# Kernel tuning notes

Measured on AMD Instinct MI355X. Metric: run time of the kernel, lower is better.

The kernel has to match this reference:

```python
import jax, jax.numpy as jnp
import numpy as np

BN_EPS = 1e-5

def binarize_ste(x):
    # sign() in forward; identity (straight-through) in backward, matching the
    # weight.data / input.data hack in BinarizeConv2d.
    return x + jax.lax.stop_gradient(jnp.sign(x) - x)


def setup_inputs() -> dict:
    key = jax.random.key(0)
    k1, k2, k3, k4 = jax.random.split(key, 4)
    N, Cin, H, W = 16, 32, 224, 224
    Cout, K = 32, 3
    x = jax.random.normal(k1, (N, Cin, H, W), dtype=jnp.float32)
    weight = jax.random.normal(k2, (Cout, Cin, K, K), dtype=jnp.float32) * 0.1
    gamma = jax.random.uniform(k3, (Cout,), dtype=jnp.float32, minval=0.5, maxval=1.5)
    beta = jax.random.normal(k4, (Cout,), dtype=jnp.float32) * 0.1
    return {"x": x, "weight": weight, "gamma": gamma, "beta": beta}


def reference(x, weight, gamma, beta):
    # BinarizeConv2d: binarize input iff C != 3, always binarize weights.
    xb = binarize_ste(x) if x.shape[1] != 3 else x
    wb = binarize_ste(weight)
    y = jax.lax.conv_general_dilated(
        xb, wb,
        window_strides=(1, 1),
        padding=((1, 1), (1, 1)),
        dimension_numbers=("NCHW", "OIHW", "NCHW"),
    )  # [N, Cout, H, W]
    # BatchNorm2d in training mode: per-channel batch statistics over (N, H, W).
    mean = jnp.mean(y, axis=(0, 2, 3))
    var = jnp.var(y, axis=(0, 2, 3))
    inv = jax.lax.rsqrt(var + BN_EPS)
    yn = (y - mean[None, :, None, None]) * inv[None, :, None, None]
    return yn * gamma[None, :, None, None] + beta[None, :, None, None]
```

## Files before the change

kernel.cpp:

```cpp
#include <hip/hip_runtime.h>
#include <stdint.h>

#define NB 16
#define CC 32
#define HH 224
#define WWID 224
#define HWS (HH*WWID)
#define NHWT (NB*HWS)
#define STRIPS (NHWT/4)
#define SPI (HWS/4)
#define SPR (WWID/4)

#define PITCH 232
#define PROWS 226
#define IMGW (PITCH*PROWS)

typedef float    f4 __attribute__((ext_vector_type(4)));
typedef unsigned u4 __attribute__((ext_vector_type(4)));
typedef unsigned u2 __attribute__((ext_vector_type(2)));

#define WS_WSIGN 0
#define WS_WNZ   2048
#define WS_BASE  4096
#define WS_FLAGW 5248
#define WS_FLAGZ 5252
#define WS_SSUM  5376
#define WS_SSQ   5632
#define WS_SCALE 5888
#define WS_SHIFT 6016
#define WS_XS    8192
#define WS_XNZ   (8192 + (size_t)NB*IMGW*4)

__global__ void pack_w(const float* __restrict__ w, unsigned* __restrict__ wsg,
                       unsigned* __restrict__ wnz, int* __restrict__ flagw,
                       int* __restrict__ baset) {
    __shared__ unsigned s_sg[288];
    __shared__ int allnz;
    if (threadIdx.x == 0) allnz = 1;
    __syncthreads();
    int k = threadIdx.x;
    if (k < 288) {
        int co = k / 9, tap = k % 9;
        unsigned bits = 0, nz = 0;
        for (int ci = 0; ci < CC; ++ci) {
            float v = w[(co * CC + ci) * 9 + tap];
            bits |= (v > 0.f ? 1u : 0u) << ci;
            nz   |= (v != 0.f ? 1u : 0u) << ci;
        }
        wsg[k] = bits; wnz[k] = nz; s_sg[k] = bits;
        if (nz != 0xffffffffu) atomicAnd(&allnz, 0);
    }
    __syncthreads();
    if (threadIdx.x == 0) *flagw = allnz;
    if (k < 288) {
        int cls = k >> 5, co = k & 31;
        int hc = cls / 3, wc = cls % 3;
        int nv = 0, corr = 0;
        #pragma unroll
        for (int kh = 0; kh < 3; ++kh)
            #pragma unroll
            for (int kw = 0; kw < 3; ++kw) {
                bool inv = (hc == 0 && kh == 0) || (hc == 2 && kh == 2) ||
                           (wc == 0 && kw == 0) || (wc == 2 && kw == 2);
                if (inv) corr += __popc(s_sg[co * 9 + kh * 3 + kw]);
                else     nv++;
            }
        baset[k] = 32 * nv + 2 * corr;
    }
}

__global__ void __launch_bounds__(256) pack_x4(const float* __restrict__ x,
                                               unsigned* __restrict__ xs,
                                               unsigned* __restrict__ xnz,
                                               int* __restrict__ flagz) {
    int t = blockIdx.x * 256 + threadIdx.x;
    int n = t / SPI, rem = t - n * SPI;
    int h = rem / SPR, w0 = (rem - h * SPR) * 4;
    const float* base = x + (size_t)n * CC * HWS + h * WWID + w0;
    unsigned b0=0,b1=0,b2=0,b3=0, z0=0,z1=0,z2=0,z3=0;
    #pragma unroll
    for (int c = 0; c < CC; ++c) {
        f4 v = __builtin_nontemporal_load((const f4*)(base + (size_t)c * HWS));
        b0 |= (v.x > 0.f ? (1u<<c) : 0u);  z0 |= (v.x != 0.f ? (1u<<c) : 0u);
        b1 |= (v.y > 0.f ? (1u<<c) : 0u);  z1 |= (v.y != 0.f ? (1u<<c) : 0u);
        b2 |= (v.z > 0.f ? (1u<<c) : 0u);  z2 |= (v.z != 0.f ? (1u<<c) : 0u);
        b3 |= (v.w > 0.f ? (1u<<c) : 0u);  z3 |= (v.w != 0.f ? (1u<<c) : 0u);
    }
    size_t d = (size_t)n * IMGW + (h + 1) * PITCH + 1 + w0;
    xs[d+0]=b0; xs[d+1]=b1; xs[d+2]=b2; xs[d+3]=b3;
    xnz[d+0]=z0; xnz[d+1]=z1; xnz[d+2]=z2; xnz[d+3]=z3;
    bool hasz = (z0 & z1 & z2 & z3) != 0xffffffffu;
    if (__any(hasz) && (threadIdx.x & 63) == 0) atomicOr(flagz, 1);
}

__device__ __forceinline__ void loadwin(const unsigned* __restrict__ p, unsigned a[6]) {
    u4 lo = *(const u4*)p;
    u2 hi = *(const u2*)(p + 4);
    a[0]=lo.x; a[1]=lo.y; a[2]=lo.z; a[3]=lo.w; a[4]=hi.x; a[5]=hi.y;
}

__device__ __forceinline__ void ad4(const unsigned a0[6], const unsigned a1[6],
                                    const unsigned a2[6],
                                    const unsigned* __restrict__ q, int ad[4]) {
    unsigned q0=q[0],q1=q[1],q2=q[2],q3=q[3],q4=q[4],q5=q[5],q6=q[6],q7=q[7],q8=q[8];
    #pragma unroll
    for (int px = 0; px < 4; ++px) {
        ad[px] = __popc(a0[px]^q0) + __popc(a0[px+1]^q1) + __popc(a0[px+2]^q2)
               + __popc(a1[px]^q3) + __popc(a1[px+1]^q4) + __popc(a1[px+2]^q5)
               + __popc(a2[px]^q6) + __popc(a2[px+1]^q7) + __popc(a2[px+2]^q8);
    }
}

__device__ __forceinline__ void y4_slowc(const unsigned a0[6], const unsigned a1[6],
                                         const unsigned a2[6], const unsigned z0[6],
                                         const unsigned z1[6], const unsigned z2[6],
                                         const unsigned* __restrict__ qs,
                                         const unsigned* __restrict__ qz, int y[4]) {
    #pragma unroll
    for (int px = 0; px < 4; ++px) {
        int am = 0, ad = 0;
        #pragma unroll
        for (int kw = 0; kw < 3; ++kw) {
            unsigned m0 = z0[px+kw] & qz[kw];
            unsigned m1 = z1[px+kw] & qz[3+kw];
            unsigned m2 = z2[px+kw] & qz[6+kw];
            am += __popc(m0) + __popc(m1) + __popc(m2);
            ad += __popc((a0[px+kw]^qs[kw])   & m0)
                + __popc((a1[px+kw]^qs[3+kw]) & m1)
                + __popc((a2[px+kw]^qs[6+kw]) & m2);
        }
        y[px] = am - 2 * ad;
    }
}

__global__ void __launch_bounds__(256, 4) convstats_fast(
        const unsigned* __restrict__ xs, const unsigned* __restrict__ wsg,
        const int* __restrict__ baset, const int* __restrict__ flagw,
        const int* __restrict__ flagz, int* __restrict__ s_sum,
        unsigned long long* __restrict__ s_sq) {
    if (!(*flagw) || *flagz) return;
    __shared__ int sb[288];
    __shared__ int ls[4][8], lq[4][8];
    for (int i = threadIdx.x; i < 288; i += 256) sb[i] = baset[i];
    __syncthreads();

    int cobase = (blockIdx.x & 3) * 8;
    int sid = (blockIdx.x >> 2) * 256 + threadIdx.x;
    int n = sid / SPI, rem = sid - n * SPI;
    int h = rem / SPR, w0 = (rem - h * SPR) * 4;
    const unsigned* ip = xs + (size_t)n * IMGW + h * PITCH + w0;

    unsigned a0[6], a1[6], a2[6];
    loadwin(ip, a0); loadwin(ip + PITCH, a1); loadwin(ip + 2 * PITCH, a2);

    int hc = (h == 0) ? 0 : ((h == HH-1) ? 6 : 3);
    int c0 = (hc + ((w0 == 0) ? 0 : 1)) * 32;
    int c1 = (hc + 1) * 32;
    int c3 = (hc + ((w0 == WWID-4) ? 2 : 1)) * 32;

    int sacc[8], qacc[8];
    #pragma unroll
    for (int u = 0; u < 8; ++u) {
        int co = cobase + u;
        int ad[4];
        ad4(a0, a1, a2, wsg + co * 9, ad);
        int y0 = sb[c0 + co] - 2 * ad[0];
        int y1 = sb[c1 + co] - 2 * ad[1];
        int y2 = sb[c1 + co] - 2 * ad[2];
        int y3 = sb[c3 + co] - 2 * ad[3];
        sacc[u] = y0 + y1 + y2 + y3;
        qacc[u] = y0*y0 + y1*y1 + y2*y2 + y3*y3;
    }

    #pragma unroll
    for (int off = 32; off; off >>= 1) {
        #pragma unroll
        for (int u = 0; u < 8; ++u) {
            sacc[u] += __shfl_down(sacc[u], off);
            qacc[u] += __shfl_down(qacc[u], off);
        }
    }
    int wid = threadIdx.x >> 6, lane = threadIdx.x & 63;
    if (lane == 0) {
        #pragma unroll
        for (int u = 0; u < 8; ++u) { ls[wid][u] = sacc[u]; lq[wid][u] = qacc[u]; }
    }
    __syncthreads();
    if (threadIdx.x < 8) {
        int u = threadIdx.x;
        int S = ls[0][u] + ls[1][u] + ls[2][u] + ls[3][u];
        long long Q = (long long)lq[0][u] + lq[1][u] + lq[2][u] + lq[3][u];
        atomicAdd(&s_sum[cobase + u], S);
        atomicAdd(&s_sq[cobase + u], (unsigned long long)Q);
    }
}

__global__ void __launch_bounds__(256, 2) convstats_slow(
        const unsigned* __restrict__ xs, const unsigned* __restrict__ xnz,
        const unsigned* __restrict__ wsg, const unsigned* __restrict__ wnz,
        const int* __restrict__ flagw, const int* __restrict__ flagz,
        int* __restrict__ s_sum, unsigned long long* __restrict__ s_sq) {
    if ((*flagw) && !(*flagz)) return;
    __shared__ int ls[4][8], lq[4][8];
    int cobase = (blockIdx.x & 3) * 8;
    int sid = (blockIdx.x >> 2) * 256 + threadIdx.x;
    int n = sid / SPI, rem = sid - n * SPI;
    int h = rem / SPR, w0 = (rem - h * SPR) * 4;
    size_t off = (size_t)n * IMGW + h * PITCH + w0;

    unsigned a0[6], a1[6], a2[6], z0[6], z1[6], z2[6];
    loadwin(xs + off, a0); loadwin(xs + off + PITCH, a1); loadwin(xs + off + 2*PITCH, a2);
    loadwin(xnz + off, z0); loadwin(xnz + off + PITCH, z1); loadwin(xnz + off + 2*PITCH, z2);

    int sacc[8], qacc[8];
    #pragma unroll
    for (int u = 0; u < 8; ++u) {
        int co = cobase + u;
        int y[4];
        y4_slowc(a0, a1, a2, z0, z1, z2, wsg + co * 9, wnz + co * 9, y);
        sacc[u] = y[0]+y[1]+y[2]+y[3];
        qacc[u] = y[0]*y[0]+y[1]*y[1]+y[2]*y[2]+y[3]*y[3];
    }
    #pragma unroll
    for (int offv = 32; offv; offv >>= 1) {
        #pragma unroll
        for (int u = 0; u < 8; ++u) {
            sacc[u] += __shfl_down(sacc[u], offv);
            qacc[u] += __shfl_down(qacc[u], offv);
        }
    }
    int wid = threadIdx.x >> 6, lane = threadIdx.x & 63;
    if (lane == 0) {
        #pragma unroll
        for (int u = 0; u < 8; ++u) { ls[wid][u] = sacc[u]; lq[wid][u] = qacc[u]; }
    }
    __syncthreads();
    if (threadIdx.x < 8) {
        int u = threadIdx.x;
        int S = ls[0][u] + ls[1][u] + ls[2][u] + ls[3][u];
        long long Q = (long long)lq[0][u] + lq[1][u] + lq[2][u] + lq[3][u];
        atomicAdd(&s_sum[cobase + u], S);
        atomicAdd(&s_sq[cobase + u], (unsigned long long)Q);
    }
}

__global__ void bfinal(const int* __restrict__ s_sum,
                       const unsigned long long* __restrict__ s_sq,
                       const float* __restrict__ gamma, const float* __restrict__ beta,
                       float* __restrict__ scale, float* __restrict__ shift) {
    int c = threadIdx.x;
    if (c >= CC) return;
    double mean = (double)s_sum[c] / (double)NHWT;
    double var  = (double)(long long)s_sq[c] / (double)NHWT - mean * mean;
    float inv = (float)(1.0 / sqrt(var + 1e-5));
    float g = gamma[c] * inv;
    scale[c] = g;
    shift[c] = beta[c] - (float)mean * g;
}

__global__ void __launch_bounds__(256, 4) convnorm_fast(
        const unsigned* __restrict__ xs, const unsigned* __restrict__ wsg,
        const int* __restrict__ baset, const int* __restrict__ flagw,
        const int* __restrict__ flagz, const float* __restrict__ scale,
        const float* __restrict__ shift, float* __restrict__ out) {
    if (!(*flagw) || *flagz) return;
    __shared__ int sb[288];
    for (int i = threadIdx.x; i < 288; i += 256) sb[i] = baset[i];
    __syncthreads();

    int cobase = (blockIdx.x & 3) * 8;
    int sid = (blockIdx.x >> 2) * 256 + threadIdx.x;
    int n = sid / SPI, rem = sid - n * SPI;
    int h = rem / SPR, w0 = (rem - h * SPR) * 4;
    const unsigned* ip = xs + (size_t)n * IMGW + h * PITCH + w0;

    unsigned a0[6], a1[6], a2[6];
    loadwin(ip, a0); loadwin(ip + PITCH, a1); loadwin(ip + 2 * PITCH, a2);

    int hc = (h == 0) ? 0 : ((h == HH-1) ? 6 : 3);
    int c0 = (hc + ((w0 == 0) ? 0 : 1)) * 32;
    int c1 = (hc + 1) * 32;
    int c3 = (hc + ((w0 == WWID-4) ? 2 : 1)) * 32;

    float* on = out + (size_t)(n * CC + cobase) * HWS + h * WWID + w0;
    #pragma unroll
    for (int u = 0; u < 8; ++u) {
        int co = cobase + u;
        int ad[4];
        ad4(a0, a1, a2, wsg + co * 9, ad);
        int y0 = sb[c0 + co] - 2 * ad[0];
        int y1 = sb[c1 + co] - 2 * ad[1];
        int y2 = sb[c1 + co] - 2 * ad[2];
        int y3 = sb[c3 + co] - 2 * ad[3];
        float sc = scale[co], sh = shift[co];
        f4 o = { fmaf((float)y0, sc, sh), fmaf((float)y1, sc, sh),
                 fmaf((float)y2, sc, sh), fmaf((float)y3, sc, sh) };
        __builtin_nontemporal_store(o, (f4*)(on + (size_t)u * HWS));
    }
}

__global__ void __launch_bounds__(256, 2) convnorm_slow(
        const unsigned* __restrict__ xs, const unsigned* __restrict__ xnz,
        const unsigned* __restrict__ wsg, const unsigned* __restrict__ wnz,
        const int* __restrict__ flagw, const int* __restrict__ flagz,
        const float* __restrict__ scale, const float* __restrict__ shift,
        float* __restrict__ out) {
    if ((*flagw) && !(*flagz)) return;
    int cobase = (blockIdx.x & 3) * 8;
    int sid = (blockIdx.x >> 2) * 256 + threadIdx.x;
    int n = sid / SPI, rem = sid - n * SPI;
    int h = rem / SPR, w0 = (rem - h * SPR) * 4;
    size_t off = (size_t)n * IMGW + h * PITCH + w0;

    unsigned a0[6], a1[6], a2[6], z0[6], z1[6], z2[6];
    loadwin(xs + off, a0); loadwin(xs + off + PITCH, a1); loadwin(xs + off + 2*PITCH, a2);
    loadwin(xnz + off, z0); loadwin(xnz + off + PITCH, z1); loadwin(xnz + off + 2*PITCH, z2);

    float* on = out + (size_t)(n * CC + cobase) * HWS + h * WWID + w0;
    #pragma unroll
    for (int u = 0; u < 8; ++u) {
        int co = cobase + u;
        int y[4];
        y4_slowc(a0, a1, a2, z0, z1, z2, wsg + co * 9, wnz + co * 9, y);
        float sc = scale[co], sh = shift[co];
        f4 o = { fmaf((float)y[0], sc, sh), fmaf((float)y[1], sc, sh),
                 fmaf((float)y[2], sc, sh), fmaf((float)y[3], sc, sh) };
        __builtin_nontemporal_store(o, (f4*)(on + (size_t)u * HWS));
    }
}

extern "C" void kernel_launch(void* const* d_in, const int* in_sizes, int n_in,
                              void* d_out, int out_size, void* d_ws, size_t ws_size,
                              hipStream_t stream) {
    const float* x     = (const float*)d_in[0];
    const float* w     = (const float*)d_in[1];
    const float* gamma = (const float*)d_in[2];
    const float* beta  = (const float*)d_in[3];
    float* out = (float*)d_out;

    char* ws = (char*)d_ws;
    unsigned* wsg            = (unsigned*)(ws + WS_WSIGN);
    unsigned* wnz            = (unsigned*)(ws + WS_WNZ);
    int* baset               = (int*)(ws + WS_BASE);
    int* flagw               = (int*)(ws + WS_FLAGW);
    int* flagz               = (int*)(ws + WS_FLAGZ);
    int* s_sum               = (int*)(ws + WS_SSUM);
    unsigned long long* s_sq = (unsigned long long*)(ws + WS_SSQ);
    float* scale             = (float*)(ws + WS_SCALE);
    float* shift             = (float*)(ws + WS_SHIFT);
    unsigned* xsb            = (unsigned*)(ws + WS_XS);
    unsigned* xzb            = (unsigned*)(ws + WS_XNZ);

    hipMemsetAsync(ws + WS_FLAGZ, 0, WS_SCALE - WS_FLAGZ, stream);
    hipMemsetAsync(ws + WS_XS, 0, (size_t)NB * IMGW * 4 * 2, stream);

    pack_w  <<<1, 320, 0, stream>>>(w, wsg, wnz, flagw, baset);
    pack_x4 <<<STRIPS / 256, 256, 0, stream>>>(x, xsb, xzb, flagz);

    int cgrid = STRIPS / 256 * 4;
    convstats_fast<<<cgrid, 256, 0, stream>>>(xsb, wsg, baset, flagw, flagz, s_sum, s_sq);
    convstats_slow<<<cgrid, 256, 0, stream>>>(xsb, xzb, wsg, wnz, flagw, flagz, s_sum, s_sq);
    bfinal  <<<1, 64, 0, stream>>>(s_sum, s_sq, gamma, beta, scale, shift);
    convnorm_fast<<<cgrid, 256, 0, stream>>>(xsb, wsg, baset, flagw, flagz, scale, shift, out);
    convnorm_slow<<<cgrid, 256, 0, stream>>>(xsb, xzb, wsg, wnz, flagw, flagz, scale, shift, out);
}
```

Measured before the change: 91.72 us.

## Drop memsets and merge fast/slow conv kernels into single launches

Removes the two hipMemsetAsync calls. The stats accumulators and the zero flag are now cleared inside pack_w, and pack_x4 writes the padding border itself, so the large padded-buffer memset is no longer needed. The separate fast and slow conv kernels are merged into one kernel per stage that branches on the flags, cutting two launches, and launch_bounds rises to 8 blocks per CU. In exchange, the merged kernel has to size its registers for the slow path too, and correctness depends on pack_w finishing its clears before pack_x4 sets flagz, which stream order provides.

New measurement: 84.50 us. -7.9%, faster.

```diff
diff --git a/kernel.cpp b/kernel.cpp
--- a/kernel.cpp
+++ b/kernel.cpp
@@ -33,10 +33,12 @@
 
 __global__ void pack_w(const float* __restrict__ w, unsigned* __restrict__ wsg,
                        unsigned* __restrict__ wnz, int* __restrict__ flagw,
-                       int* __restrict__ baset) {
+                       int* __restrict__ baset, int* __restrict__ s_sum,
+                       unsigned long long* __restrict__ s_sq, int* __restrict__ flagz) {
     __shared__ unsigned s_sg[288];
     __shared__ int allnz;
-    if (threadIdx.x == 0) allnz = 1;
+    if (threadIdx.x == 0) { allnz = 1; *flagz = 0; }
+    if (threadIdx.x < CC) { s_sum[threadIdx.x] = 0; s_sq[threadIdx.x] = 0ull; }
     __syncthreads();
     int k = threadIdx.x;
     if (k < 288) {
@@ -86,9 +88,28 @@
         b2 |= (v.z > 0.f ? (1u<<c) : 0u);  z2 |= (v.z != 0.f ? (1u<<c) : 0u);
         b3 |= (v.w > 0.f ? (1u<<c) : 0u);  z3 |= (v.w != 0.f ? (1u<<c) : 0u);
     }
-    size_t d = (size_t)n * IMGW + (h + 1) * PITCH + 1 + w0;
+    size_t rowb = (size_t)n * IMGW + (h + 1) * PITCH;
+    size_t d = rowb + 1 + w0;
     xs[d+0]=b0; xs[d+1]=b1; xs[d+2]=b2; xs[d+3]=b3;
     xnz[d+0]=z0; xnz[d+1]=z1; xnz[d+2]=z2; xnz[d+3]=z3;
+
+    if (w0 == 0)        { xs[rowb] = 0;       xnz[rowb] = 0; }
+    if (w0 == WWID - 4) { xs[rowb + 225] = 0; xnz[rowb + 225] = 0; }
+    if (h == 0) {
+        size_t tr = (size_t)n * IMGW;
+        #pragma unroll
+        for (int j = 0; j < 4; ++j) { xs[tr + 1 + w0 + j] = 0; xnz[tr + 1 + w0 + j] = 0; }
+        if (w0 == 0)        { xs[tr] = 0;       xnz[tr] = 0; }
+        if (w0 == WWID - 4) { xs[tr + 225] = 0; xnz[tr + 225] = 0; }
+    }
+    if (h == HH - 1) {
+        size_t br = (size_t)n * IMGW + (size_t)(PROWS - 1) * PITCH;
+        #pragma unroll
+        for (int j = 0; j < 4; ++j) { xs[br + 1 + w0 + j] = 0; xnz[br + 1 + w0 + j] = 0; }
+        if (w0 == 0)        { xs[br] = 0;       xnz[br] = 0; }
+        if (w0 == WWID - 4) { xs[br + 225] = 0; xnz[br + 225] = 0; }
+    }
+
     bool hasz = (z0 & z1 & z2 & z3) != 0xffffffffu;
     if (__any(hasz) && (threadIdx.x & 63) == 0) atomicOr(flagz, 1);
 }
@@ -133,100 +154,64 @@
     }
 }
 
-__global__ void __launch_bounds__(256, 4) convstats_fast(
-        const unsigned* __restrict__ xs, const unsigned* __restrict__ wsg,
+__global__ void __launch_bounds__(256, 8) convstats(
+        const unsigned* __restrict__ xs, const unsigned* __restrict__ xnz,
+        const unsigned* __restrict__ wsg, const unsigned* __restrict__ wnz,
         const int* __restrict__ baset, const int* __restrict__ flagw,
         const int* __restrict__ flagz, int* __restrict__ s_sum,
         unsigned long long* __restrict__ s_sq) {
-    if (!(*flagw) || *flagz) return;
     __shared__ int sb[288];
     __shared__ int ls[4][8], lq[4][8];
     for (int i = threadIdx.x; i < 288; i += 256) sb[i] = baset[i];
     __syncthreads();
 
-    int cobase = (blockIdx.x & 3) * 8;
-    int sid = (blockIdx.x >> 2) * 256 + threadIdx.x;
-    int n = sid / SPI, rem = sid - n * SPI;
-    int h = rem / SPR, w0 = (rem - h * SPR) * 4;
-    const unsigned* ip = xs + (size_t)n * IMGW + h * PITCH + w0;
-
-    unsigned a0[6], a1[6], a2[6];
-    loadwin(ip, a0); loadwin(ip + PITCH, a1); loadwin(ip + 2 * PITCH, a2);
-
-    int hc = (h == 0) ? 0 : ((h == HH-1) ? 6 : 3);
-    int c0 = (hc + ((w0 == 0) ? 0 : 1)) * 32;
-    int c1 = (hc + 1) * 32;
-    int c3 = (hc + ((w0 == WWID-4) ? 2 : 1)) * 32;
-
-    int sacc[8], qacc[8];
-    #pragma unroll
-    for (int u = 0; u < 8; ++u) {
-        int co = cobase + u;
-        int ad[4];
-        ad4(a0, a1, a2, wsg + co * 9, ad);
-        int y0 = sb[c0 + co] - 2 * ad[0];
-        int y1 = sb[c1 + co] - 2 * ad[1];
-        int y2 = sb[c1 + co] - 2 * ad[2];
-        int y3 = sb[c3 + co] - 2 * ad[3];
-        sacc[u] = y0 + y1 + y2 + y3;
-        qacc[u] = y0*y0 + y1*y1 + y2*y2 + y3*y3;
-    }
-
-    #pragma unroll
-    for (int off = 32; off; off >>= 1) {
-        #pragma unroll
-        for (int u = 0; u < 8; ++u) {
-            sacc[u] += __shfl_down(sacc[u], off);
-            qacc[u] += __shfl_down(qacc[u], off);
-        }
-    }
-    int wid = threadIdx.x >> 6, lane = threadIdx.x & 63;
-    if (lane == 0) {
-        #pragma unroll
-        for (int u = 0; u < 8; ++u) { ls[wid][u] = sacc[u]; lq[wid][u] = qacc[u]; }
-    }
-    __syncthreads();
-    if (threadIdx.x < 8) {
-        int u = threadIdx.x;
-        int S = ls[0][u] + ls[1][u] + ls[2][u] + ls[3][u];
-        long long Q = (long long)lq[0][u] + lq[1][u] + lq[2][u] + lq[3][u];
-        atomicAdd(&s_sum[cobase + u], S);
-        atomicAdd(&s_sq[cobase + u], (unsigned long long)Q);
-    }
-}
-
-__global__ void __launch_bounds__(256, 2) convstats_slow(
-        const unsigned* __restrict__ xs, const unsigned* __restrict__ xnz,
-        const unsigned* __restrict__ wsg, const unsigned* __restrict__ wnz,
-        const int* __restrict__ flagw, const int* __restrict__ flagz,
-        int* __restrict__ s_sum, unsigned long long* __restrict__ s_sq) {
-    if ((*flagw) && !(*flagz)) return;
-    __shared__ int ls[4][8], lq[4][8];
     int cobase = (blockIdx.x & 3) * 8;
     int sid = (blockIdx.x >> 2) * 256 + threadIdx.x;
     int n = sid / SPI, rem = sid - n * SPI;
     int h = rem / SPR, w0 = (rem - h * SPR) * 4;
     size_t off = (size_t)n * IMGW + h * PITCH + w0;
 
-    unsigned a0[6], a1[6], a2[6], z0[6], z1[6], z2[6];
+    unsigned a0[6], a1[6], a2[6];
     loadwin(xs + off, a0); loadwin(xs + off + PITCH, a1); loadwin(xs + off + 2*PITCH, a2);
-    loadwin(xnz + off, z0); loadwin(xnz + off + PITCH, z1); loadwin(xnz + off + 2*PITCH, z2);
 
     int sacc[8], qacc[8];
+    bool fast = (*flagw != 0) && (*flagz == 0);
+    if (fast) {
+        int hc = (h == 0) ? 0 : ((h == HH-1) ? 6 : 3);
+        int c0 = (hc + ((w0 == 0) ? 0 : 1)) * 32;
+        int c1 = (hc + 1) * 32;
+        int c3 = (hc + ((w0 == WWID-4) ? 2 : 1)) * 32;
+        #pragma unroll
+        for (int u = 0; u < 8; ++u) {
+            int co = cobase + u;
+            int ad[4];
+            ad4(a0, a1, a2, wsg + co * 9, ad);
+            int y0 = sb[c0 + co] - 2 * ad[0];
+            int y1 = sb[c1 + co] - 2 * ad[1];
+            int y2 = sb[c1 + co] - 2 * ad[2];
+            int y3 = sb[c3 + co] - 2 * ad[3];
+            sacc[u] = y0 + y1 + y2 + y3;
+            qacc[u] = y0*y0 + y1*y1 + y2*y2 + y3*y3;
+        }
+    } else {
+        unsigned z0[6], z1[6], z2[6];
+        loadwin(xnz + off, z0); loadwin(xnz + off + PITCH, z1); loadwin(xnz + off + 2*PITCH, z2);
+        #pragma unroll
+        for (int u = 0; u < 8; ++u) {
+            int co = cobase + u;
+            int y[4];
+            y4_slowc(a0, a1, a2, z0, z1, z2, wsg + co * 9, wnz + co * 9, y);
+            sacc[u] = y[0]+y[1]+y[2]+y[3];
+            qacc[u] = y[0]*y[0]+y[1]*y[1]+y[2]*y[2]+y[3]*y[3];
+        }
+    }
+
     #pragma unroll
-    for (int u = 0; u < 8; ++u) {
-        int co = cobase + u;
-        int y[4];
-        y4_slowc(a0, a1, a2, z0, z1, z2, wsg + co * 9, wnz + co * 9, y);
-        sacc[u] = y[0]+y[1]+y[2]+y[3];
-        qacc[u] = y[0]*y[0]+y[1]*y[1]+y[2]*y[2]+y[3]*y[3];
-    }
-    #pragma unroll
-    for (int offv = 32; offv; offv >>= 1) {
-        #pragma unroll
-        for (int u = 0; u < 8; ++u) {
-            sacc[u] += __shfl_down(sacc[u], offv);
-            qacc[u] += __shfl_down(qacc[u], offv);
+    for (int off2 = 32; off2; off2 >>= 1) {
+        #pragma unroll
+        for (int u = 0; u < 8; ++u) {
+            sacc[u] += __shfl_down(sacc[u], off2);
+            qacc[u] += __shfl_down(qacc[u], off2);
         }
     }
     int wid = threadIdx.x >> 6, lane = threadIdx.x & 63;
@@ -258,74 +243,59 @@
     shift[c] = beta[c] - (float)mean * g;
 }
 
-__global__ void __launch_bounds__(256, 4) convnorm_fast(
-        const unsigned* __restrict__ xs, const unsigned* __restrict__ wsg,
+__global__ void __launch_bounds__(256, 8) convnorm(
+        const unsigned* __restrict__ xs, const unsigned* __restrict__ xnz,
+        const unsigned* __restrict__ wsg, const unsigned* __restrict__ wnz,
         const int* __restrict__ baset, const int* __restrict__ flagw,
         const int* __restrict__ flagz, const float* __restrict__ scale,
         const float* __restrict__ shift, float* __restrict__ out) {
-    if (!(*flagw) || *flagz) return;
     __shared__ int sb[288];
     for (int i = threadIdx.x; i < 288; i += 256) sb[i] = baset[i];
     __syncthreads();
 
-    int cobase = (blockIdx.x & 3) * 8;
-    int sid = (blockIdx.x >> 2) * 256 + threadIdx.x;
-    int n = sid / SPI, rem = sid - n * SPI;
-    int h = rem / SPR, w0 = (rem - h * SPR) * 4;
-    const unsigned* ip = xs + (size_t)n * IMGW + h * PITCH + w0;
-
-    unsigned a0[6], a1[6], a2[6];
-    loadwin(ip, a0); loadwin(ip + PITCH, a1); loadwin(ip + 2 * PITCH, a2);
-
-    int hc = (h == 0) ? 0 : ((h == HH-1) ? 6 : 3);
-    int c0 = (hc + ((w0 == 0) ? 0 : 1)) * 32;
-    int c1 = (hc + 1) * 32;
-    int c3 = (hc + ((w0 == WWID-4) ? 2 : 1)) * 32;
-
-    float* on = out + (size_t)(n * CC + cobase) * HWS + h * WWID + w0;
-    #pragma unroll
-    for (int u = 0; u < 8; ++u) {
-        int co = cobase + u;
-        int ad[4];
-        ad4(a0, a1, a2, wsg + co * 9, ad);
-        int y0 = sb[c0 + co] - 2 * ad[0];
-        int y1 = sb[c1 + co] - 2 * ad[1];
-        int y2 = sb[c1 + co] - 2 * ad[2];
-        int y3 = sb[c3 + co] - 2 * ad[3];
-        float sc = scale[co], sh = shift[co];
-        f4 o = { fmaf((float)y0, sc, sh), fmaf((float)y1, sc, sh),
-                 fmaf((float)y2, sc, sh), fmaf((float)y3, sc, sh) };
-        __builtin_nontemporal_store(o, (f4*)(on + (size_t)u * HWS));
-    }
-}
-
-__global__ void __launch_bounds__(256, 2) convnorm_slow(
-        const unsigned* __restrict__ xs, const unsigned* __restrict__ xnz,
-        const unsigned* __restrict__ wsg, const unsigned* __restrict__ wnz,
-        const int* __restrict__ flagw, const int* __restrict__ flagz,
-        const float* __restrict__ scale, const float* __restrict__ shift,
-        float* __restrict__ out) {
-    if ((*flagw) && !(*flagz)) return;
     int cobase = (blockIdx.x & 3) * 8;
     int sid = (blockIdx.x >> 2) * 256 + threadIdx.x;
     int n = sid / SPI, rem = sid - n * SPI;
     int h = rem / SPR, w0 = (rem - h * SPR) * 4;
     size_t off = (size_t)n * IMGW + h * PITCH + w0;
 
-    unsigned a0[6], a1[6], a2[6], z0[6], z1[6], z2[6];
+    unsigned a0[6], a1[6], a2[6];
     loadwin(xs + off, a0); loadwin(xs + off + PITCH, a1); loadwin(xs + off + 2*PITCH, a2);
-    loadwin(xnz + off, z0); loadwin(xnz + off + PITCH, z1); loadwin(xnz + off + 2*PITCH, z2);
 
     float* on = out + (size_t)(n * CC + cobase) * HWS + h * WWID + w0;
-    #pragma unroll
-    for (int u = 0; u < 8; ++u) {
-        int co = cobase + u;
-        int y[4];
-        y4_slowc(a0, a1, a2, z0, z1, z2, wsg + co * 9, wnz + co * 9, y);
-        float sc = scale[co], sh = shift[co];
-        f4 o = { fmaf((float)y[0], sc, sh), fmaf((float)y[1], sc, sh),
-                 fmaf((float)y[2], sc, sh), fmaf((float)y[3], sc, sh) };
-        __builtin_nontemporal_store(o, (f4*)(on + (size_t)u * HWS));
+    bool fast = (*flagw != 0) && (*flagz == 0);
+    if (fast) {
+        int hc = (h == 0) ? 0 : ((h == HH-1) ? 6 : 3);
+        int c0 = (hc + ((w0 == 0) ? 0 : 1)) * 32;
+        int c1 = (hc + 1) * 32;
+        int c3 = (hc + ((w0 == WWID-4) ? 2 : 1)) * 32;
+        #pragma unroll
+        for (int u = 0; u < 8; ++u) {
+            int co = cobase + u;
+            int ad[4];
+            ad4(a0, a1, a2, wsg + co * 9, ad);
+            int y0 = sb[c0 + co] - 2 * ad[0];
+            int y1 = sb[c1 + co] - 2 * ad[1];
+            int y2 = sb[c1 + co] - 2 * ad[2];
+            int y3 = sb[c3 + co] - 2 * ad[3];
+            float sc = scale[co], sh = shift[co];
+            f4 o = { fmaf((float)y0, sc, sh), fmaf((float)y1, sc, sh),
+                     fmaf((float)y2, sc, sh), fmaf((float)y3, sc, sh) };
+            __builtin_nontemporal_store(o, (f4*)(on + (size_t)u * HWS));
+        }
+    } else {
+        unsigned z0[6], z1[6], z2[6];
+        loadwin(xnz + off, z0); loadwin(xnz + off + PITCH, z1); loadwin(xnz + off + 2*PITCH, z2);
+        #pragma unroll
+        for (int u = 0; u < 8; ++u) {
+            int co = cobase + u;
+            int y[4];
+            y4_slowc(a0, a1, a2, z0, z1, z2, wsg + co * 9, wnz + co * 9, y);
+            float sc = scale[co], sh = shift[co];
+            f4 o = { fmaf((float)y[0], sc, sh), fmaf((float)y[1], sc, sh),
+                     fmaf((float)y[2], sc, sh), fmaf((float)y[3], sc, sh) };
+            __builtin_nontemporal_store(o, (f4*)(on + (size_t)u * HWS));
+        }
     }
 }
 
@@ -351,16 +321,11 @@
     unsigned* xsb            = (unsigned*)(ws + WS_XS);
     unsigned* xzb            = (unsigned*)(ws + WS_XNZ);
 
-    hipMemsetAsync(ws + WS_FLAGZ, 0, WS_SCALE - WS_FLAGZ, stream);
-    hipMemsetAsync(ws + WS_XS, 0, (size_t)NB * IMGW * 4 * 2, stream);
-
-    pack_w  <<<1, 320, 0, stream>>>(w, wsg, wnz, flagw, baset);
-    pack_x4 <<<STRIPS / 256, 256, 0, stream>>>(x, xsb, xzb, flagz);
-
     int cgrid = STRIPS / 256 * 4;
-    convstats_fast<<<cgrid, 256, 0, stream>>>(xsb, wsg, baset, flagw, flagz, s_sum, s_sq);
-    convstats_slow<<<cgrid, 256, 0, stream>>>(xsb, xzb, wsg, wnz, flagw, flagz, s_sum, s_sq);
-    bfinal  <<<1, 64, 0, stream>>>(s_sum, s_sq, gamma, beta, scale, shift);
-    convnorm_fast<<<cgrid, 256, 0, stream>>>(xsb, wsg, baset, flagw, flagz, scale, shift, out);
-    convnorm_slow<<<cgrid, 256, 0, stream>>>(xsb, xzb, wsg, wnz, flagw, flagz, scale, shift, out);
-}
+    pack_w   <<<1, 320, 0, stream>>>(w, wsg, wnz, flagw, baset, s_sum, s_sq, flagz);
+    pack_x4  <<<STRIPS / 256, 256, 0, stream>>>(x, xsb, xzb, flagz);
+    convstats<<<cgrid, 256, 0, stream>>>(xsb, xzb, wsg, wnz, baset, flagw, flagz, s_sum, s_sq);
+    bfinal   <<<1, 64, 0, stream>>>(s_sum, s_sq, gamma, beta, scale, shift);
+    convnorm <<<cgrid, 256, 0, stream>>>(xsb, xzb, wsg, wnz, baset, flagw, flagz,
+                                         scale, shift, out);
+}
```
